# Kernel tuning notes

Measured on AMD Instinct MI355X. Metric: run time of the kernel, lower is better.

## Reference

```python
import jax, jax.numpy as jnp
import numpy as np

N = 102400   # nodes (256 graphs x 400 nodes)
E = 819200   # edges (avg degree 8)
D = 120      # input_channels
H = 200      # hidden_channels
CC = D + H   # 320 concat dim
L = 400      # nodes per graph (hardcoded view in forward)
B = N // L   # 256 graphs
STEPS = 8
NETYPES = 2


def conv1d(x, w, b):
    # x: [B, C, L], w: [O, I, K] -> [B, O, L-K+1] (VALID, like torch Conv1d)
    y = jax.lax.conv_general_dilated(x, w, (1,), 'VALID',
                                     dimension_numbers=('NCH', 'OIH', 'NCH'))
    return y + b[None, :, None]


def maxpool1d(x, k, s):
    return jax.lax.reduce_window(x, -jnp.inf, jax.lax.max,
                                 (1, 1, k), (1, 1, s), 'VALID')


def setup_inputs():
    key = jax.random.key(0)
    ks = jax.random.split(key, 32)
    g = lambda i, shape, s=0.05: jax.random.normal(ks[i], shape, jnp.float32) * s
    return dict(
        x=g(0, (N, D), 1.0),
        edge_index=jax.random.randint(ks[1], (2, E), 0, N),
        edge_types=jax.random.randint(ks[2], (E,), 0, NETYPES),
        ggnn_W=g(3, (NETYPES, H, H)), ggnn_b=g(4, (NETYPES, H)),
        gru_Wih=g(5, (3 * H, H)), gru_Whh=g(6, (3 * H, H)),
        gru_bih=g(7, (3 * H,)), gru_bhh=g(8, (3 * H,)),
        conv1_w=g(9, (H, H, 3)), conv1_b=g(10, (H,)),
        conv2_w=g(11, (H, H, 1)), conv2_b=g(12, (H,)),
        cconv1_w=g(13, (CC, CC, 3)), cconv1_b=g(14, (CC,)),
        cconv2_w=g(15, (CC, CC, 1)), cconv2_b=g(16, (CC,)),
        mlp_y_w=g(17, (256, H)), mlp_y_b=g(18, (256,)),
        mlp_z_w=g(19, (256, CC)), mlp_z_b=g(20, (256,)),
        ml_l1_w=g(21, (128, 256)), ml_l1_b=g(22, (128,)),
        ml_f1_w=g(23, (64, 128)), ml_f1_b=g(24, (64,)),
        ml_f2_w=g(25, (128, 64)), ml_f2_b=g(26, (128,)),
        cls_w=g(27, (2, 128)), cls_b=g(28, (2,)),
    )


def reference(x, edge_index, edge_types, ggnn_W, ggnn_b, gru_Wih, gru_Whh,
              gru_bih, gru_bhh, conv1_w, conv1_b, conv2_w, conv2_b,
              cconv1_w, cconv1_b, cconv2_w, cconv2_b, mlp_y_w, mlp_y_b,
              mlp_z_w, mlp_z_b, ml_l1_w, ml_l1_b, ml_f1_w, ml_f1_b,
              ml_f2_w, ml_f2_b, cls_w, cls_b):
    src, dst = edge_index[0], edge_index[1]
    emask = [(edge_types == e).astype(x.dtype)[:, None] for e in range(NETYPES)]

    # --- GatedGraphConv: zero-pad feats to H, then 8 steps of
    #     per-etype linear -> gather(src) -> scatter-add(dst) -> GRUCell ---
    h = jnp.pad(x, ((0, 0), (0, H - D)))  # [N, H]
    for _ in range(STEPS):
        a = jnp.zeros((N, H), x.dtype)
        for e in range(NETYPES):
            Wh = h @ ggnn_W[e].T + ggnn_b[e]           # [N, H]
            msg = Wh[src] * emask[e]                    # [E, H]
            a = a + jax.ops.segment_sum(msg, dst, num_segments=N)
        gi = a @ gru_Wih.T + gru_bih                    # [N, 3H]
        gh = h @ gru_Whh.T + gru_bhh                    # [N, 3H]
        ir, iz, inn = jnp.split(gi, 3, axis=-1)
        hr, hz, hn = jnp.split(gh, 3, axis=-1)
        r = jax.nn.sigmoid(ir + hr)
        z = jax.nn.sigmoid(iz + hz)
        n = jnp.tanh(inn + r * hn)
        h = (1.0 - z) * n + z * h
    outputs = h                                         # [N, H]

    # --- conv/pool readout (dropout = identity at eval) ---
    c_i = jnp.concatenate([x, outputs], axis=1).reshape(B, L, CC)
    h_i = outputs.reshape(B, L, H)

    Y1 = maxpool1d(jax.nn.relu(conv1d(h_i.transpose(0, 2, 1), conv1_w, conv1_b)), 3, 2)
    Y2 = maxpool1d(jax.nn.relu(conv1d(Y1, conv2_w, conv2_b)), 2, 2).transpose(0, 2, 1)  # [B,99,H]
    Z1 = maxpool1d(jax.nn.relu(conv1d(c_i.transpose(0, 2, 1), cconv1_w, cconv1_b)), 3, 2)
    Z2 = maxpool1d(jax.nn.relu(conv1d(Z1, cconv2_w, cconv2_b)), 2, 2).transpose(0, 2, 1)  # [B,99,CC]

    before_avg = (Y2 @ mlp_y_w.T + mlp_y_b) * (Z2 @ mlp_z_w.T + mlp_z_b)  # [B,99,256]
    avg = before_avg.mean(axis=1)                                          # [B,256]

    # --- MetricLearningModel head ---
    h1 = jax.nn.relu(avg @ ml_l1_w.T + ml_l1_b)                 # [B,128]
    hf = jax.nn.relu(h1 @ ml_f1_w.T + ml_f1_b)                  # [B,64]
    hf = jax.nn.relu(hf @ ml_f2_w.T + ml_f2_b)                  # [B,128] embedding
    logits = hf @ cls_w.T + cls_b                               # [B,2]
    return logits, hf
```

## Files before the change

kernel.cpp:

```cpp
#include <hip/hip_runtime.h>
#include <hip/hip_bf16.h>
#include <cstdint>
#include <cstddef>

static constexpr int NN = 102400;
static constexpr int EE = 819200;
static constexpr int DD = 120;
static constexpr int HH = 200;
static constexpr int LL = 400;
static constexpr int BB = 256;
static constexpr int NSTEPS = 8;

typedef __attribute__((ext_vector_type(8))) short short8;
typedef __attribute__((ext_vector_type(4))) float f32x4;

__device__ __forceinline__ unsigned short f2bf(float f) {
  union { float f; unsigned u; } v; v.f = f;
  return (unsigned short)((v.u + 0x7fffu + ((v.u >> 16) & 1u)) >> 16);
}
__device__ __forceinline__ float bf2f(unsigned short s) {
  union { unsigned u; float f; } v; v.u = ((unsigned)s) << 16; return v.f;
}

template<int AMODE, int ASRC, int OBF, int RELU>
__global__ __launch_bounds__(256) void gemm_mfma(
    const void* __restrict__ Asrc, const float* __restrict__ X2,
    const short* __restrict__ WP, const float* __restrict__ bias,
    void* __restrict__ Cdst, int M, int Nout, int K, int KT)
{
  __shared__ short Asm[4096];
  __shared__ short Bsm[4096];
  const int tid = threadIdx.x;
  const int row0 = blockIdx.y * 128;
  const int col0 = blockIdx.x * 128;

  f32x4 acc[4][4];
#pragma unroll
  for (int mi = 0; mi < 4; mi++)
#pragma unroll
    for (int ni = 0; ni < 4; ni++) acc[mi][ni] = (f32x4){0.f, 0.f, 0.f, 0.f};

  const int r = tid & 15;
  const int kgl = (tid >> 4) & 3;
  const int ghalf = tid >> 6;
  const int w = tid >> 6, l = tid & 63;
  const int wr = w >> 1, wc = w & 1;

  for (int t = 0; t < KT; t++) {
#pragma unroll
    for (int half = 0; half < 2; half++) {
      const int g = ghalf + half * 4;
      int row = row0 + g * 16 + r;
      if (row >= M) row = M - 1;
      const int k0 = t * 32 + kgl * 8;
      short8 sv;
      if (AMODE == 0 && ASRC == 1) {
        if (k0 < K) {
          sv = *reinterpret_cast<const short8*>(
              (const unsigned short*)Asrc + (size_t)row * K + k0);
        } else {
#pragma unroll
          for (int j = 0; j < 8; j++) sv[j] = 0;
        }
      } else {
        const float* p = nullptr;
        bool ok = true;
        if (AMODE == 0) {
          if (k0 < K) p = (const float*)Asrc + (size_t)row * K + k0;
          else ok = false;
        } else if (AMODE == 1) {
          if (k0 < K) {
            const int b = row / 398, tt = row - b * 398;
            const int tap = k0 / 200, i0 = k0 - tap * 200;
            p = (const float*)Asrc + ((size_t)(b * 400 + tt + tap)) * 200 + i0;
          } else ok = false;
        } else {
          const int b = row / 398, tt = row - b * 398;
          const int tap = k0 / 320, c0 = k0 - tap * 320;
          const int node = b * 400 + tt + tap;
          if (c0 < 120) p = X2 + (size_t)node * 120 + c0;
          else p = (const float*)Asrc + (size_t)node * 200 + (c0 - 120);
        }
        float v[8];
        if (ok) {
          const float4 x0 = *reinterpret_cast<const float4*>(p);
          const float4 x1 = *reinterpret_cast<const float4*>(p + 4);
          v[0] = x0.x; v[1] = x0.y; v[2] = x0.z; v[3] = x0.w;
          v[4] = x1.x; v[5] = x1.y; v[6] = x1.z; v[7] = x1.w;
        } else {
#pragma unroll
          for (int j = 0; j < 8; j++) v[j] = 0.f;
        }
#pragma unroll
        for (int j = 0; j < 8; j++) sv[j] = (short)f2bf(v[j]);
      }
      *reinterpret_cast<short8*>(&Asm[(g * 64 + (tid & 63)) * 8]) = sv;
    }
    {
      const size_t wbase = ((size_t)blockIdx.x * KT + t) * 4096;
#pragma unroll
      for (int it = 0; it < 2; it++) {
        const int idx = it * 256 + tid;
        *reinterpret_cast<short8*>(&Bsm[idx * 8]) =
            *reinterpret_cast<const short8*>(WP + wbase + (size_t)idx * 8);
      }
    }
    __syncthreads();
    short8 af[4], bfr[4];
#pragma unroll
    for (int mi = 0; mi < 4; mi++)
      af[mi] = *reinterpret_cast<const short8*>(&Asm[((wr * 4 + mi) * 64 + l) * 8]);
#pragma unroll
    for (int ni = 0; ni < 4; ni++)
      bfr[ni] = *reinterpret_cast<const short8*>(&Bsm[((wc * 4 + ni) * 64 + l) * 8]);
#pragma unroll
    for (int mi = 0; mi < 4; mi++)
#pragma unroll
      for (int ni = 0; ni < 4; ni++)
        acc[mi][ni] = __builtin_amdgcn_mfma_f32_16x16x32_bf16(
            af[mi], bfr[ni], acc[mi][ni], 0, 0, 0);
    __syncthreads();
  }

#pragma unroll
  for (int mi = 0; mi < 4; mi++)
#pragma unroll
    for (int ni = 0; ni < 4; ni++) {
      const int col = col0 + wc * 64 + ni * 16 + (l & 15);
      if (col < Nout) {
        const float bb = bias ? bias[col] : 0.f;
        const int rbase = row0 + wr * 64 + mi * 16 + ((l >> 4) << 2);
#pragma unroll
        for (int q = 0; q < 4; q++) {
          const int row = rbase + q;
          if (row < M) {
            float val = acc[mi][ni][q] + bb;
            if (RELU) val = fmaxf(val, 0.f);
            if (OBF)
              ((unsigned short*)Cdst)[(size_t)row * Nout + col] = f2bf(val);
            else
              ((float*)Cdst)[(size_t)row * Nout + col] = val;
          }
        }
      }
    }
}

__global__ void pack_w(const float* __restrict__ W, short* __restrict__ WP,
                       int Nout, int K, int Ntp, int Kp, int CIN) {
  const int KT = Kp >> 5;
  const int total = (Ntp >> 7) * KT * 512;
  const int u = blockIdx.x * 256 + threadIdx.x;
  if (u >= total) return;
  const int l = u & 63;
  const int g = (u >> 6) & 7;
  const int T = (u >> 9) % KT;
  const int ct = (u >> 9) / KT;
  const int n = ct * 128 + g * 16 + (l & 15);
  const int kb = T * 32 + ((l >> 4) << 3);
  short8 sv;
#pragma unroll
  for (int j = 0; j < 8; j++) {
    const int k = kb + j;
    float v = 0.f;
    if (n < Nout && k < K) {
      if (CIN > 0) {
        const int kw = k / CIN, i = k - kw * CIN;
        v = W[((size_t)n * CIN + i) * 3 + kw];
      } else {
        v = W[(size_t)n * K + k];
      }
    }
    sv[j] = (short)f2bf(v);
  }
  *reinterpret_cast<short8*>(&WP[(size_t)u * 8]) = sv;
}

__global__ void fill_kernel(float* __restrict__ p, int n, float v) {
  const int t = blockIdx.x * 256 + threadIdx.x;
  if (t < n) p[t] = v;
}

__global__ void pad_h_kernel(const float* __restrict__ x, float* __restrict__ h) {
  const int t = blockIdx.x * 256 + threadIdx.x;
  if (t >= NN * HH) return;
  const int n = t / HH, j = t - n * HH;
  h[t] = (j < DD) ? x[(size_t)n * DD + j] : 0.0f;
}

__global__ void hist_kernel(const int* __restrict__ ei, int* __restrict__ cnt) {
  const int e = blockIdx.x * 256 + threadIdx.x;
  if (e < EE) atomicAdd(&cnt[ei[EE + e]], 1);
}
__global__ void scan1_kernel(const int* __restrict__ cnt, int* __restrict__ ex,
                             int* __restrict__ bsum) {
  __shared__ int sm[256];
  const int tid = threadIdx.x;
  const int i = blockIdx.x * 256 + tid;
  const int v = cnt[i];
  sm[tid] = v; __syncthreads();
  for (int off = 1; off < 256; off <<= 1) {
    int t = (tid >= off) ? sm[tid - off] : 0;
    __syncthreads();
    sm[tid] += t;
    __syncthreads();
  }
  ex[i] = sm[tid] - v;
  if (tid == 255) bsum[blockIdx.x] = sm[255];
}
__global__ void scan2_kernel(int* __restrict__ bsum, int nb) {
  if (threadIdx.x == 0 && blockIdx.x == 0) {
    int run = 0;
    for (int b = 0; b < nb; b++) { int t = bsum[b]; bsum[b] = run; run += t; }
  }
}
__global__ void scan3_kernel(const int* __restrict__ ex, const int* __restrict__ bsum,
                             int* __restrict__ rowptr) {
  const int i = blockIdx.x * 256 + threadIdx.x;
  if (i < NN) rowptr[i] = ex[i] + bsum[i >> 8];
  if (i == 0) rowptr[NN] = EE;
}
__global__ void fillcsr_kernel(const int* __restrict__ ei, const int* __restrict__ et,
                               const int* __restrict__ rowptr, int* __restrict__ fcur,
                               int* __restrict__ eidx) {
  const int e = blockIdx.x * 256 + threadIdx.x;
  if (e >= EE) return;
  const int d = ei[EE + e];
  const int pos = atomicAdd(&fcur[d], 1);
  eidx[rowptr[d] + pos] = (ei[e] << 1) | (et[e] & 1);
}

__global__ void agg_kernel(const unsigned short* __restrict__ Whb,
                           const int* __restrict__ rowptr,
                           const int* __restrict__ eidx,
                           const float* __restrict__ gb,
                           unsigned short* __restrict__ abf) {
  const int nid = blockIdx.x * 4 + (threadIdx.x >> 6);
  const int lane = threadIdx.x & 63;
  if (nid >= NN) return;
  const int beg = rowptr[nid], end = rowptr[nid + 1];
  float a0 = 0.f, a1 = 0.f, a2 = 0.f, a3 = 0.f, c0 = 0.f, c1 = 0.f;
  const unsigned int* W32 = (const unsigned int*)Whb;
  for (int e = beg; e < end; e++) {
    const int pe = eidx[e];
    const int src = pe >> 1, ty = pe & 1;
    if (ty) c1 += 1.f; else c0 += 1.f;
    const unsigned int* wrow = W32 + (size_t)src * 200 + ty * 100;
    const unsigned int u0 = wrow[lane];
    a0 += bf2f((unsigned short)(u0 & 0xffffu));
    a1 += bf2f((unsigned short)(u0 >> 16));
    if (lane < 36) {
      const unsigned int u1 = wrow[64 + lane];
      a2 += bf2f((unsigned short)(u1 & 0xffffu));
      a3 += bf2f((unsigned short)(u1 >> 16));
    }
  }
  unsigned int* A32 = (unsigned int*)abf;
  const int cA = 2 * lane, cB = cA + 1;
  a0 += c0 * gb[cA] + c1 * gb[200 + cA];
  a1 += c0 * gb[cB] + c1 * gb[200 + cB];
  A32[(size_t)nid * 100 + lane] =
      (unsigned int)f2bf(a0) | ((unsigned int)f2bf(a1) << 16);
  if (lane < 36) {
    const int cC = 128 + 2 * lane, cD = cC + 1;
    a2 += c0 * gb[cC] + c1 * gb[200 + cC];
    a3 += c0 * gb[cD] + c1 * gb[200 + cD];
    A32[(size_t)nid * 100 + 64 + lane] =
        (unsigned int)f2bf(a2) | ((unsigned int)f2bf(a3) << 16);
  }
}

__global__ void gru_kernel(const unsigned short* __restrict__ gi,
                           const unsigned short* __restrict__ gh,
                           float* __restrict__ h, int n0, int NC) {
  const int t = blockIdx.x * 256 + threadIdx.x;
  if (t >= NC * HH) return;
  const int ln = t / HH, j = t - ln * HH;
  const unsigned short* gir = gi + (size_t)ln * 600;
  const unsigned short* ghr = gh + (size_t)ln * 600;
  const float ir = bf2f(gir[j]), iz = bf2f(gir[200 + j]), inn = bf2f(gir[400 + j]);
  const float hr = bf2f(ghr[j]), hz = bf2f(ghr[200 + j]), hn = bf2f(ghr[400 + j]);
  const float rr = 1.0f / (1.0f + expf(-(ir + hr)));
  const float zz = 1.0f / (1.0f + expf(-(iz + hz)));
  const float nn = tanhf(inn + rr * hn);
  const size_t hi = (size_t)(n0 + ln) * HH + j;
  h[hi] = (1.0f - zz) * nn + zz * h[hi];
}

__global__ void pool_kernel(const float* __restrict__ src, float* __restrict__ dst,
                            int nb, int Lin, int Lout, int C, int win) {
  const size_t t = (size_t)blockIdx.x * 256 + threadIdx.x;
  const size_t tot = (size_t)nb * Lout * C;
  if (t >= tot) return;
  const int c = (int)(t % C);
  const size_t bp = t / C;
  const int p = (int)(bp % Lout);
  const int b = (int)(bp / Lout);
  const float* s0 = src + ((size_t)b * Lin + 2 * p) * C + c;
  float v = s0[0];
  for (int q = 1; q < win; q++) v = fmaxf(v, s0[(size_t)q * C]);
  dst[t] = v;
}

__global__ void prodmean_kernel(const float* __restrict__ y, const float* __restrict__ z,
                                float* __restrict__ avg, int g0, int nb) {
  const int t = blockIdx.x * 256 + threadIdx.x;
  if (t >= nb * 256) return;
  const int b = t >> 8, j = t & 255;
  const float* yr = y + (size_t)b * 99 * 256 + j;
  const float* zr = z + (size_t)b * 99 * 256 + j;
  float sum = 0.0f;
  for (int p = 0; p < 99; p++) sum += yr[(size_t)p * 256] * zr[(size_t)p * 256];
  avg[(size_t)(g0 + b) * 256 + j] = sum * (1.0f / 99.0f);
}

extern "C" void kernel_launch(void* const* d_in, const int* in_sizes, int n_in,
                              void* d_out, int out_size, void* d_ws, size_t ws_size,
                              hipStream_t stream) {
  const float* x       = (const float*)d_in[0];
  const int*   ei      = (const int*)d_in[1];
  const int*   et      = (const int*)d_in[2];
  const float* ggnn_W  = (const float*)d_in[3];
  const float* ggnn_b  = (const float*)d_in[4];
  const float* gru_Wih = (const float*)d_in[5];
  const float* gru_Whh = (const float*)d_in[6];
  const float* gru_bih = (const float*)d_in[7];
  const float* gru_bhh = (const float*)d_in[8];
  const float* conv1_w = (const float*)d_in[9];
  const float* conv1_b = (const float*)d_in[10];
  const float* conv2_w = (const float*)d_in[11];
  const float* conv2_b = (const float*)d_in[12];
  const float* cconv1_w = (const float*)d_in[13];
  const float* cconv1_b = (const float*)d_in[14];
  const float* cconv2_w = (const float*)d_in[15];
  const float* cconv2_b = (const float*)d_in[16];
  const float* mlp_y_w = (const float*)d_in[17];
  const float* mlp_y_b = (const float*)d_in[18];
  const float* mlp_z_w = (const float*)d_in[19];
  const float* mlp_z_b = (const float*)d_in[20];
  const float* ml_l1_w = (const float*)d_in[21];
  const float* ml_l1_b = (const float*)d_in[22];
  const float* ml_f1_w = (const float*)d_in[23];
  const float* ml_f1_b = (const float*)d_in[24];
  const float* ml_f2_w = (const float*)d_in[25];
  const float* ml_f2_b = (const float*)d_in[26];
  const float* cls_w   = (const float*)d_in[27];
  const float* cls_b   = (const float*)d_in[28];
  float* out = (float*)d_out;

  char* base = (char*)d_ws;
  size_t off = 0;
  auto alloc = [&](size_t bytes) { char* p = base + off; off += (bytes + 15) & ~(size_t)15; return p; };
  float* h            = (float*)alloc(81920000);
  unsigned short* abf = (unsigned short*)alloc(40960000);
  int* cnt    = (int*)alloc(409600);
  int* ex     = (int*)alloc(409600);
  int* bsum   = (int*)alloc(1600);
  int* rowptr = (int*)alloc(409604);
  int* fcur   = (int*)alloc(409600);
  int* eidx   = (int*)alloc(3276800);
  short* WPg   = (short*)alloc(229376);
  short* WPwih = (short*)alloc(286720);
  short* WPwhh = (short*)alloc(286720);
  short* WPc1  = (short*)alloc(311296);
  short* WPcc1 = (short*)alloc(737280);
  short* WPc2  = (short*)alloc(114688);
  short* WPcc2 = (short*)alloc(245760);
  short* WPmy  = (short*)alloc(114688);
  short* WPmz  = (short*)alloc(163840);
  short* WPl1  = (short*)alloc(65536);
  short* WPf1  = (short*)alloc(32768);
  short* WPf2  = (short*)alloc(16384);
  short* WPcls = (short*)alloc(32768);
  float* avg = (float*)alloc(262144);
  float* h1b = (float*)alloc(131072);
  float* hf1 = (float*)alloc(65536);
  char* dynb = base + off;
  const size_t dyn_bytes = (ws_size > off) ? (ws_size - off) : 0;

  const size_t WHB_BYTES = 81920000;
  int CH2 = (int)((dyn_bytes / 2400) & ~(size_t)127);
  if (CH2 > NN) CH2 = NN;
  int G = 0;
  { const int cand[4] = {256, 128, 64, 32};
    for (int i = 0; i < 4; i++)
      if ((size_t)cand[i] * 1222240 <= dyn_bytes) { G = cand[i]; break; } }

  const int fill_blocks = (out_size + 255) / 256;
  if (dyn_bytes < WHB_BYTES || CH2 < 128 || G == 0) {
    fill_kernel<<<fill_blocks, 256, 0, stream>>>(out, out_size,
                                                 -(float)(ws_size >> 20));
    return;
  }
  fill_kernel<<<fill_blocks, 256, 0, stream>>>(out, out_size, 1.0e4f);

  pad_h_kernel<<<80000, 256, 0, stream>>>(x, h);
  hipMemsetAsync(cnt, 0, 409600, stream);
  hipMemsetAsync(fcur, 0, 409600, stream);
  hist_kernel<<<3200, 256, 0, stream>>>(ei, cnt);
  scan1_kernel<<<400, 256, 0, stream>>>(cnt, ex, bsum);
  scan2_kernel<<<1, 64, 0, stream>>>(bsum, 400);
  scan3_kernel<<<400, 256, 0, stream>>>(ex, bsum, rowptr);
  fillcsr_kernel<<<3200, 256, 0, stream>>>(ei, et, rowptr, fcur, eidx);

  auto packs = [&](const float* W, short* WP, int Nout, int K, int Ntp, int Kp, int CIN) {
    const int total = (Ntp >> 7) * (Kp >> 5) * 512;
    pack_w<<<(total + 255) / 256, 256, 0, stream>>>(W, WP, Nout, K, Ntp, Kp, CIN);
  };
  packs(ggnn_W,  WPg,   400, 200, 512, 224, 0);
  packs(gru_Wih, WPwih, 600, 200, 640, 224, 0);
  packs(gru_Whh, WPwhh, 600, 200, 640, 224, 0);
  packs(conv1_w, WPc1,  200, 600, 256, 608, 200);
  packs(cconv1_w,WPcc1, 320, 960, 384, 960, 320);
  packs(conv2_w, WPc2,  200, 200, 256, 224, 0);
  packs(cconv2_w,WPcc2, 320, 320, 384, 320, 0);
  packs(mlp_y_w, WPmy,  256, 200, 256, 224, 0);
  packs(mlp_z_w, WPmz,  256, 320, 256, 320, 0);
  packs(ml_l1_w, WPl1,  128, 256, 128, 256, 0);
  packs(ml_f1_w, WPf1,   64, 128, 128, 128, 0);
  packs(ml_f2_w, WPf2,  128,  64, 128,  64, 0);
  packs(cls_w,   WPcls,   2, 128, 128, 128, 0);

  unsigned short* Whb = (unsigned short*)dynb;
  unsigned short* gi  = (unsigned short*)dynb;
  unsigned short* gh  = gi + (size_t)CH2 * 600;
  for (int step = 0; step < NSTEPS; step++) {
    gemm_mfma<0, 0, 1, 0><<<dim3(4, 800), 256, 0, stream>>>(
        h, nullptr, WPg, nullptr, Whb, NN, 400, 200, 7);
    agg_kernel<<<25600, 256, 0, stream>>>(Whb, rowptr, eidx, ggnn_b, abf);
    for (int n0 = 0; n0 < NN; n0 += CH2) {
      const int NC = (NN - n0 < CH2) ? (NN - n0) : CH2;
      const int gy = (NC + 127) / 128;
      gemm_mfma<0, 1, 1, 0><<<dim3(5, gy), 256, 0, stream>>>(
          abf + (size_t)n0 * HH, nullptr, WPwih, gru_bih, gi, NC, 600, 200, 7);
      gemm_mfma<0, 0, 1, 0><<<dim3(5, gy), 256, 0, stream>>>(
          h + (size_t)n0 * HH, nullptr, WPwhh, gru_bhh, gh, NC, 600, 200, 7);
      gru_kernel<<<(NC * HH + 255) / 256, 256, 0, stream>>>(gi, gh, h, n0, NC);
    }
  }

  float* b0  = (float*)dynb;
  float* b1  = b0 + (size_t)G * 127360;
  float* b2  = b1 + (size_t)G * 63360;
  float* y2c = b2 + (size_t)G * 63360;
  float* z2c = y2c + (size_t)G * 19800;

  for (int g0 = 0; g0 < BB; g0 += G) {
    const float* hc = h + (size_t)g0 * LL * HH;
    const float* xc = x + (size_t)g0 * LL * DD;
    const int M1 = G * 398, M2 = G * 198, M3 = G * 99;
    const int gy1 = (M1 + 127) / 128, gy2 = (M2 + 127) / 128, gy3 = (M3 + 127) / 128;
    gemm_mfma<1, 0, 0, 1><<<dim3(2, gy1), 256, 0, stream>>>(
        hc, nullptr, WPc1, conv1_b, b0, M1, 200, 600, 19);
    pool_kernel<<<(int)(((size_t)G * 198 * 200 + 255) / 256), 256, 0, stream>>>(
        b0, b1, G, 398, 198, 200, 3);
    gemm_mfma<0, 0, 0, 1><<<dim3(2, gy2), 256, 0, stream>>>(
        b1, nullptr, WPc2, conv2_b, b2, M2, 200, 200, 7);
    pool_kernel<<<(int)(((size_t)G * 99 * 200 + 255) / 256), 256, 0, stream>>>(
        b2, y2c, G, 198, 99, 200, 2);
    gemm_mfma<2, 0, 0, 1><<<dim3(3, gy1), 256, 0, stream>>>(
        hc, xc, WPcc1, cconv1_b, b0, M1, 320, 960, 30);
    pool_kernel<<<(int)(((size_t)G * 198 * 320 + 255) / 256), 256, 0, stream>>>(
        b0, b1, G, 398, 198, 320, 3);
    gemm_mfma<0, 0, 0, 1><<<dim3(3, gy2), 256, 0, stream>>>(
        b1, nullptr, WPcc2, cconv2_b, b2, M2, 320, 320, 10);
    pool_kernel<<<(int)(((size_t)G * 99 * 320 + 255) / 256), 256, 0, stream>>>(
        b2, z2c, G, 198, 99, 320, 2);
    gemm_mfma<0, 0, 0, 0><<<dim3(2, gy3), 256, 0, stream>>>(
        y2c, nullptr, WPmy, mlp_y_b, b0, M3, 256, 200, 7);
    gemm_mfma<0, 0, 0, 0><<<dim3(2, gy3), 256, 0, stream>>>(
        z2c, nullptr, WPmz, mlp_z_b, b1, M3, 256, 320, 10);
    prodmean_kernel<<<(G * 256 + 255) / 256, 256, 0, stream>>>(b0, b1, avg, g0, G);
  }

  gemm_mfma<0, 0, 0, 1><<<dim3(1, 2), 256, 0, stream>>>(
      avg, nullptr, WPl1, ml_l1_b, h1b, 256, 128, 256, 8);
  gemm_mfma<0, 0, 0, 1><<<dim3(1, 2), 256, 0, stream>>>(
      h1b, nullptr, WPf1, ml_f1_b, hf1, 256, 64, 128, 4);
  gemm_mfma<0, 0, 0, 1><<<dim3(1, 2), 256, 0, stream>>>(
      hf1, nullptr, WPf2, ml_f2_b, out + 512, 256, 128, 64, 2);
  gemm_mfma<0, 0, 0, 0><<<dim3(1, 2), 256, 0, stream>>>(
      out + 512, nullptr, WPcls, cls_b, out, 256, 2, 128, 4);
}
```

Before: 5.773 ms.

## Aggregate before transform and fuse GGNN+GRU into one GEMM with gated epilogue

```diff
diff --git a/kernel.cpp b/kernel.cpp
--- a/kernel.cpp
+++ b/kernel.cpp
@@ -22,11 +22,14 @@
   union { unsigned u; float f; } v; v.u = ((unsigned)s) << 16; return v.f;
 }
 
-template<int AMODE, int ASRC, int OBF, int RELU>
+template<int AMODE, int ASRC, int OBF, int RELU, int EPI>
 __global__ __launch_bounds__(256) void gemm_mfma(
-    const void* __restrict__ Asrc, const float* __restrict__ X2,
+    const void* __restrict__ Asrc, const void* __restrict__ A2,
     const short* __restrict__ WP, const float* __restrict__ bias,
-    void* __restrict__ Cdst, int M, int Nout, int K, int KT)
+    void* __restrict__ Cdst, int M, int Nout, int K, int KT,
+    const float* __restrict__ tt0, const float* __restrict__ tt1,
+    const float* __restrict__ cnt2, float* __restrict__ hout,
+    unsigned short* __restrict__ hbout)
 {
   __shared__ short Asm[4096];
   __shared__ short Bsm[4096];
@@ -54,45 +57,66 @@
       if (row >= M) row = M - 1;
       const int k0 = t * 32 + kgl * 8;
       short8 sv;
+      bool direct = false;
       if (AMODE == 0 && ASRC == 1) {
         if (k0 < K) {
           sv = *reinterpret_cast<const short8*>(
               (const unsigned short*)Asrc + (size_t)row * K + k0);
-        } else {
-#pragma unroll
-          for (int j = 0; j < 8; j++) sv[j] = 0;
-        }
-      } else {
-        const float* p = nullptr;
-        bool ok = true;
-        if (AMODE == 0) {
-          if (k0 < K) p = (const float*)Asrc + (size_t)row * K + k0;
-          else ok = false;
-        } else if (AMODE == 1) {
-          if (k0 < K) {
-            const int b = row / 398, tt = row - b * 398;
-            const int tap = k0 / 200, i0 = k0 - tap * 200;
-            p = (const float*)Asrc + ((size_t)(b * 400 + tt + tap)) * 200 + i0;
-          } else ok = false;
-        } else {
+          direct = true;
+        }
+      } else if (AMODE == 1) {
+        if (k0 < K) {
+          const int b = row / 398, tt = row - b * 398;
+          const int tap = k0 / 200, i0 = k0 - tap * 200;
+          sv = *reinterpret_cast<const short8*>(
+              (const unsigned short*)Asrc + ((size_t)(b * 400 + tt + tap)) * 200 + i0);
+          direct = true;
+        }
+      } else if (AMODE == 3) {
+        if (k0 < 400) {
+          sv = *reinterpret_cast<const short8*>(
+              (const unsigned short*)Asrc + (size_t)row * 400 + k0);
+          direct = true;
+        } else if (k0 < 600) {
+          sv = *reinterpret_cast<const short8*>(
+              (const unsigned short*)A2 + (size_t)row * 200 + (k0 - 400));
+          direct = true;
+        }
+      } else if (AMODE == 2) {
+        if (k0 < K) {
           const int b = row / 398, tt = row - b * 398;
           const int tap = k0 / 320, c0 = k0 - tap * 320;
           const int node = b * 400 + tt + tap;
-          if (c0 < 120) p = X2 + (size_t)node * 120 + c0;
-          else p = (const float*)Asrc + (size_t)node * 200 + (c0 - 120);
-        }
-        float v[8];
-        if (ok) {
+          if (c0 < 120) {
+            const float* p = (const float*)A2 + (size_t)node * 120 + c0;
+            const float4 x0 = *reinterpret_cast<const float4*>(p);
+            const float4 x1 = *reinterpret_cast<const float4*>(p + 4);
+            sv[0] = (short)f2bf(x0.x); sv[1] = (short)f2bf(x0.y);
+            sv[2] = (short)f2bf(x0.z); sv[3] = (short)f2bf(x0.w);
+            sv[4] = (short)f2bf(x1.x); sv[5] = (short)f2bf(x1.y);
+            sv[6] = (short)f2bf(x1.z); sv[7] = (short)f2bf(x1.w);
+            direct = true;
+          } else {
+            sv = *reinterpret_cast<const short8*>(
+                (const unsigned short*)Asrc + (size_t)node * 200 + (c0 - 120));
+            direct = true;
+          }
+        }
+      } else {
+        if (k0 < K) {
+          const float* p = (const float*)Asrc + (size_t)row * K + k0;
           const float4 x0 = *reinterpret_cast<const float4*>(p);
           const float4 x1 = *reinterpret_cast<const float4*>(p + 4);
-          v[0] = x0.x; v[1] = x0.y; v[2] = x0.z; v[3] = x0.w;
-          v[4] = x1.x; v[5] = x1.y; v[6] = x1.z; v[7] = x1.w;
-        } else {
-#pragma unroll
-          for (int j = 0; j < 8; j++) v[j] = 0.f;
-        }
-#pragma unroll
-        for (int j = 0; j < 8; j++) sv[j] = (short)f2bf(v[j]);
+          sv[0] = (short)f2bf(x0.x); sv[1] = (short)f2bf(x0.y);
+          sv[2] = (short)f2bf(x0.z); sv[3] = (short)f2bf(x0.w);
+          sv[4] = (short)f2bf(x1.x); sv[5] = (short)f2bf(x1.y);
+          sv[6] = (short)f2bf(x1.z); sv[7] = (short)f2bf(x1.w);
+          direct = true;
+        }
+      }
+      if (!direct) {
+#pragma unroll
+        for (int j = 0; j < 8; j++) sv[j] = 0;
       }
       *reinterpret_cast<short8*>(&Asm[(g * 64 + (tid & 63)) * 8]) = sv;
     }
@@ -122,28 +146,61 @@
     __syncthreads();
   }
 
-#pragma unroll
-  for (int mi = 0; mi < 4; mi++)
-#pragma unroll
-    for (int ni = 0; ni < 4; ni++) {
-      const int col = col0 + wc * 64 + ni * 16 + (l & 15);
-      if (col < Nout) {
-        const float bb = bias ? bias[col] : 0.f;
-        const int rbase = row0 + wr * 64 + mi * 16 + ((l >> 4) << 2);
-#pragma unroll
-        for (int q = 0; q < 4; q++) {
-          const int row = rbase + q;
-          if (row < M) {
-            float val = acc[mi][ni][q] + bb;
-            if (RELU) val = fmaxf(val, 0.f);
-            if (OBF)
-              ((unsigned short*)Cdst)[(size_t)row * Nout + col] = f2bf(val);
-            else
-              ((float*)Cdst)[(size_t)row * Nout + col] = val;
+  if (EPI == 0) {
+#pragma unroll
+    for (int mi = 0; mi < 4; mi++)
+#pragma unroll
+      for (int ni = 0; ni < 4; ni++) {
+        const int col = col0 + wc * 64 + ni * 16 + (l & 15);
+        if (col < Nout) {
+          const float bbv = bias ? bias[col] : 0.f;
+          const int rbase = row0 + wr * 64 + mi * 16 + ((l >> 4) << 2);
+#pragma unroll
+          for (int q = 0; q < 4; q++) {
+            const int row = rbase + q;
+            if (row < M) {
+              float val = acc[mi][ni][q] + bbv;
+              if (RELU) val = fmaxf(val, 0.f);
+              if (OBF)
+                ((unsigned short*)Cdst)[(size_t)row * Nout + col] = f2bf(val);
+              else
+                ((float*)Cdst)[(size_t)row * Nout + col] = val;
+            }
+          }
+        }
+      }
+  } else {
+    const int g = l & 3;
+#pragma unroll
+    for (int mi = 0; mi < 4; mi++) {
+#pragma unroll
+      for (int q = 0; q < 4; q++) {
+        const int row = row0 + wr * 64 + mi * 16 + ((l >> 4) << 2) + q;
+        const float2 cc = *reinterpret_cast<const float2*>(cnt2 + (size_t)row * 2);
+#pragma unroll
+        for (int ni = 0; ni < 4; ni++) {
+          const int col = col0 + wc * 64 + ni * 16 + (l & 15);
+          float val = acc[mi][ni][q] + bias[col] + cc.x * tt0[col] + cc.y * tt1[col];
+          float av;
+          if (g == 0 || g == 1) av = 1.f / (1.f + expf(-val));
+          else av = val;
+          const float x1 = __shfl_xor(av, 1);
+          const float x2 = __shfl_xor(av, 2);
+          const float x3 = __shfl_xor(av, 3);
+          if (g == 2 && col < 800) {
+            const int ch = col >> 2;
+            const float nv = tanhf(av + x2 * x1);
+            float hold;
+            if (hout) hold = hout[(size_t)row * 200 + ch];
+            else hold = bf2f(((const unsigned short*)A2)[(size_t)row * 200 + ch]);
+            const float hnew = (1.f - x3) * nv + x3 * hold;
+            if (hout) hout[(size_t)row * 200 + ch] = hnew;
+            hbout[(size_t)row * 200 + ch] = f2bf(hnew);
           }
         }
       }
     }
+  }
 }
 
 __global__ void pack_w(const float* __restrict__ W, short* __restrict__ WP,
@@ -181,11 +238,14 @@
   if (t < n) p[t] = v;
 }
 
-__global__ void pad_h_kernel(const float* __restrict__ x, float* __restrict__ h) {
+__global__ void pad_h_kernel(const float* __restrict__ x, float* __restrict__ h,
+                             unsigned short* __restrict__ hb) {
   const int t = blockIdx.x * 256 + threadIdx.x;
   if (t >= NN * HH) return;
   const int n = t / HH, j = t - n * HH;
-  h[t] = (j < DD) ? x[(size_t)n * DD + j] : 0.0f;
+  const float v = (j < DD) ? x[(size_t)n * DD + j] : 0.0f;
+  if (h) h[t] = v;
+  hb[t] = f2bf(v);
 }
 
 __global__ void hist_kernel(const int* __restrict__ ei, int* __restrict__ cnt) {
@@ -229,62 +289,94 @@
   const int pos = atomicAdd(&fcur[d], 1);
   eidx[rowptr[d] + pos] = (ei[e] << 1) | (et[e] & 1);
 }
-
-__global__ void agg_kernel(const unsigned short* __restrict__ Whb,
-                           const int* __restrict__ rowptr,
-                           const int* __restrict__ eidx,
-                           const float* __restrict__ gb,
-                           unsigned short* __restrict__ abf) {
+__global__ void count_kernel(const int* __restrict__ ei, const int* __restrict__ et,
+                             float* __restrict__ cnt2) {
+  const int e = blockIdx.x * 256 + threadIdx.x;
+  if (e >= EE) return;
+  atomicAdd(&cnt2[(size_t)ei[EE + e] * 2 + (et[e] & 1)], 1.0f);
+}
+
+__global__ void wcat2_kernel(const float* __restrict__ gw, float* __restrict__ W2) {
+  const int t = blockIdx.x * 256 + threadIdx.x;
+  if (t >= 400 * 200) return;
+  const int m = t / 200, j = t - m * 200;
+  const int ty = (m < 200) ? 0 : 1;
+  const int kk = m - ty * 200;
+  W2[t] = gw[(size_t)ty * 40000 + j * 200 + kk];
+}
+__global__ void ta_kernel(const float* __restrict__ wih, const float* __restrict__ gb,
+                          float* __restrict__ ta) {
+  const int o = blockIdx.x * 256 + threadIdx.x;
+  if (o >= 1200) return;
+  const int which = o / 600, oo = o - which * 600;
+  float s = 0.f;
+  for (int j = 0; j < 200; j++) s += wih[(size_t)oo * 200 + j] * gb[which * 200 + j];
+  ta[o] = s;
+}
+__global__ void wfd_kernel(const float* __restrict__ M1, const float* __restrict__ whh,
+                           float* __restrict__ WFD) {
+  const int t = blockIdx.x * 256 + threadIdx.x;
+  if (t >= 800 * 600) return;
+  const int c = t / 600, k = t - c * 600;
+  const int ch = c >> 2, g = c & 3;
+  float v = 0.f;
+  if (g == 0) v = (k < 400) ? M1[(size_t)ch * 400 + k] : whh[(size_t)ch * 200 + (k - 400)];
+  else if (g == 1) v = (k < 400) ? M1[(size_t)(200 + ch) * 400 + k]
+                                 : whh[(size_t)(200 + ch) * 200 + (k - 400)];
+  else if (g == 2) v = (k < 400) ? M1[(size_t)(400 + ch) * 400 + k] : 0.f;
+  else v = (k < 400) ? 0.f : whh[(size_t)(400 + ch) * 200 + (k - 400)];
+  WFD[t] = v;
+}
+__global__ void bbtt_kernel(const float* __restrict__ bih, const float* __restrict__ bhh,
+                            const float* __restrict__ ta, float* __restrict__ bb,
+                            float* __restrict__ tt0, float* __restrict__ tt1) {
+  const int c = blockIdx.x * 256 + threadIdx.x;
+  if (c >= 896) return;
+  const int ch = c >> 2, g = c & 3;
+  float b = 0.f, t0 = 0.f, t1 = 0.f;
+  if (ch < 200) {
+    if (g == 0) b = bih[ch] + bhh[ch];
+    else if (g == 1) b = bih[200 + ch] + bhh[200 + ch];
+    else if (g == 2) b = bih[400 + ch];
+    else b = bhh[400 + ch];
+    if (g < 3) { t0 = ta[g * 200 + ch]; t1 = ta[600 + g * 200 + ch]; }
+  }
+  bb[c] = b; tt0[c] = t0; tt1[c] = t1;
+}
+
+__global__ void gather_kernel(const unsigned short* __restrict__ hb,
+                              const int* __restrict__ rowptr,
+                              const int* __restrict__ eidx,
+                              unsigned short* __restrict__ s) {
   const int nid = blockIdx.x * 4 + (threadIdx.x >> 6);
-  const int lane = threadIdx.x & 63;
+  const int l = threadIdx.x & 63;
   if (nid >= NN) return;
   const int beg = rowptr[nid], end = rowptr[nid + 1];
-  float a0 = 0.f, a1 = 0.f, a2 = 0.f, a3 = 0.f, c0 = 0.f, c1 = 0.f;
-  const unsigned int* W32 = (const unsigned int*)Whb;
+  float a00 = 0, a01 = 0, a10 = 0, a11 = 0;
+  float b00 = 0, b01 = 0, b10 = 0, b11 = 0;
+  const unsigned int* H32 = (const unsigned int*)hb;
   for (int e = beg; e < end; e++) {
     const int pe = eidx[e];
     const int src = pe >> 1, ty = pe & 1;
-    if (ty) c1 += 1.f; else c0 += 1.f;
-    const unsigned int* wrow = W32 + (size_t)src * 200 + ty * 100;
-    const unsigned int u0 = wrow[lane];
-    a0 += bf2f((unsigned short)(u0 & 0xffffu));
-    a1 += bf2f((unsigned short)(u0 >> 16));
-    if (lane < 36) {
-      const unsigned int u1 = wrow[64 + lane];
-      a2 += bf2f((unsigned short)(u1 & 0xffffu));
-      a3 += bf2f((unsigned short)(u1 >> 16));
-    }
-  }
-  unsigned int* A32 = (unsigned int*)abf;
-  const int cA = 2 * lane, cB = cA + 1;
-  a0 += c0 * gb[cA] + c1 * gb[200 + cA];
-  a1 += c0 * gb[cB] + c1 * gb[200 + cB];
-  A32[(size_t)nid * 100 + lane] =
-      (unsigned int)f2bf(a0) | ((unsigned int)f2bf(a1) << 16);
-  if (lane < 36) {
-    const int cC = 128 + 2 * lane, cD = cC + 1;
-    a2 += c0 * gb[cC] + c1 * gb[200 + cC];
-    a3 += c0 * gb[cD] + c1 * gb[200 + cD];
-    A32[(size_t)nid * 100 + 64 + lane] =
-        (unsigned int)f2bf(a2) | ((unsigned int)f2bf(a3) << 16);
-  }
-}
-
-__global__ void gru_kernel(const unsigned short* __restrict__ gi,
-                           const unsigned short* __restrict__ gh,
-                           float* __restrict__ h, int n0, int NC) {
-  const int t = blockIdx.x * 256 + threadIdx.x;
-  if (t >= NC * HH) return;
-  const int ln = t / HH, j = t - ln * HH;
-  const unsigned short* gir = gi + (size_t)ln * 600;
-  const unsigned short* ghr = gh + (size_t)ln * 600;
-  const float ir = bf2f(gir[j]), iz = bf2f(gir[200 + j]), inn = bf2f(gir[400 + j]);
-  const float hr = bf2f(ghr[j]), hz = bf2f(ghr[200 + j]), hn = bf2f(ghr[400 + j]);
-  const float rr = 1.0f / (1.0f + expf(-(ir + hr)));
-  const float zz = 1.0f / (1.0f + expf(-(iz + hz)));
-  const float nn = tanhf(inn + rr * hn);
-  const size_t hi = (size_t)(n0 + ln) * HH + j;
-  h[hi] = (1.0f - zz) * nn + zz * h[hi];
+    const unsigned int* hr = H32 + (size_t)src * 100;
+    const unsigned int u0 = hr[l];
+    unsigned int u1 = 0;
+    if (l < 36) u1 = hr[64 + l];
+    const float f0 = bf2f((unsigned short)(u0 & 0xffffu));
+    const float f1 = bf2f((unsigned short)(u0 >> 16));
+    const float f2 = bf2f((unsigned short)(u1 & 0xffffu));
+    const float f3 = bf2f((unsigned short)(u1 >> 16));
+    if (ty == 0) { a00 += f0; a01 += f1; a10 += f2; a11 += f3; }
+    else         { b00 += f0; b01 += f1; b10 += f2; b11 += f3; }
+  }
+  unsigned int* S32 = (unsigned int*)s;
+  const size_t rb = (size_t)nid * 200;
+  S32[rb + l] = (unsigned int)f2bf(a00) | ((unsigned int)f2bf(a01) << 16);
+  S32[rb + 100 + l] = (unsigned int)f2bf(b00) | ((unsigned int)f2bf(b01) << 16);
+  if (l < 36) {
+    S32[rb + 64 + l] = (unsigned int)f2bf(a10) | ((unsigned int)f2bf(a11) << 16);
+    S32[rb + 164 + l] = (unsigned int)f2bf(b10) | ((unsigned int)f2bf(b11) << 16);
+  }
 }
 
 __global__ void pool_kernel(const float* __restrict__ src, float* __restrict__ dst,
@@ -351,17 +443,14 @@
   char* base = (char*)d_ws;
   size_t off = 0;
   auto alloc = [&](size_t bytes) { char* p = base + off; off += (bytes + 15) & ~(size_t)15; return p; };
-  float* h            = (float*)alloc(81920000);
-  unsigned short* abf = (unsigned short*)alloc(40960000);
-  int* cnt    = (int*)alloc(409600);
-  int* ex     = (int*)alloc(409600);
-  int* bsum   = (int*)alloc(1600);
-  int* rowptr = (int*)alloc(409604);
-  int* fcur   = (int*)alloc(409600);
-  int* eidx   = (int*)alloc(3276800);
-  short* WPg   = (short*)alloc(229376);
-  short* WPwih = (short*)alloc(286720);
-  short* WPwhh = (short*)alloc(286720);
+  unsigned short* s   = (unsigned short*)alloc(81920000);
+  unsigned short* hb1 = (unsigned short*)alloc(40960000);
+  unsigned short* hb0 = (unsigned short*)alloc(40960000);
+  int* eidx    = (int*)alloc(3276800);
+  int* rowptr  = (int*)alloc(409604);
+  float* cnt2  = (float*)alloc(819200);
+  short* WPF   = (short*)alloc(1089536);
+  short* WPwc  = (short*)alloc(229376);
   short* WPc1  = (short*)alloc(311296);
   short* WPcc1 = (short*)alloc(737280);
   short* WPc2  = (short*)alloc(114688);
@@ -372,44 +461,60 @@
   short* WPf1  = (short*)alloc(32768);
   short* WPf2  = (short*)alloc(16384);
   short* WPcls = (short*)alloc(32768);
+  float* bb  = (float*)alloc(3584);
+  float* tt0 = (float*)alloc(3584);
+  float* tt1 = (float*)alloc(3584);
   float* avg = (float*)alloc(262144);
   float* h1b = (float*)alloc(131072);
   float* hf1 = (float*)alloc(65536);
-  char* dynb = base + off;
-  const size_t dyn_bytes = (ws_size > off) ? (ws_size - off) : 0;
-
-  const size_t WHB_BYTES = 81920000;
-  int CH2 = (int)((dyn_bytes / 2400) & ~(size_t)127);
-  if (CH2 > NN) CH2 = NN;
-  int G = 0;
-  { const int cand[4] = {256, 128, 64, 32};
-    for (int i = 0; i < 4; i++)
-      if ((size_t)cand[i] * 1222240 <= dyn_bytes) { G = cand[i]; break; } }
+  const size_t persist = off;
+  float* h = (float*)alloc(81920000);
+  const bool has_h = (ws_size >= off);
 
   const int fill_blocks = (out_size + 255) / 256;
-  if (dyn_bytes < WHB_BYTES || CH2 < 128 || G == 0) {
+  if (ws_size < persist) {
     fill_kernel<<<fill_blocks, 256, 0, stream>>>(out, out_size,
                                                  -(float)(ws_size >> 20));
     return;
   }
+  float* hptr = has_h ? h : nullptr;
+
+  char* ali = (char*)s;
+  float* Wcat2 = (float*)(ali);
+  float* M1f   = (float*)(ali + 320000);
+  float* WFD   = (float*)(ali + 1280000);
+  float* ta    = (float*)(ali + 3200000);
+  int* cnt     = (int*)(ali + 3204800);
+  int* ex      = (int*)(ali + 3614400);
+  int* bsum    = (int*)(ali + 4024000);
+  int* fcur    = (int*)(ali + 4025600);
+
   fill_kernel<<<fill_blocks, 256, 0, stream>>>(out, out_size, 1.0e4f);
 
-  pad_h_kernel<<<80000, 256, 0, stream>>>(x, h);
+  pad_h_kernel<<<80000, 256, 0, stream>>>(x, hptr, hb0);
   hipMemsetAsync(cnt, 0, 409600, stream);
   hipMemsetAsync(fcur, 0, 409600, stream);
+  hipMemsetAsync(cnt2, 0, 819200, stream);
   hist_kernel<<<3200, 256, 0, stream>>>(ei, cnt);
   scan1_kernel<<<400, 256, 0, stream>>>(cnt, ex, bsum);
   scan2_kernel<<<1, 64, 0, stream>>>(bsum, 400);
   scan3_kernel<<<400, 256, 0, stream>>>(ex, bsum, rowptr);
   fillcsr_kernel<<<3200, 256, 0, stream>>>(ei, et, rowptr, fcur, eidx);
+  count_kernel<<<3200, 256, 0, stream>>>(ei, et, cnt2);
 
   auto packs = [&](const float* W, short* WP, int Nout, int K, int Ntp, int Kp, int CIN) {
     const int total = (Ntp >> 7) * (Kp >> 5) * 512;
     pack_w<<<(total + 255) / 256, 256, 0, stream>>>(W, WP, Nout, K, Ntp, Kp, CIN);
   };
-  packs(ggnn_W,  WPg,   400, 200, 512, 224, 0);
-  packs(gru_Wih, WPwih, 600, 200, 640, 224, 0);
-  packs(gru_Whh, WPwhh, 600, 200, 640, 224, 0);
+  wcat2_kernel<<<313, 256, 0, stream>>>(ggnn_W, Wcat2);
+  packs(Wcat2, WPwc, 400, 200, 512, 224, 0);
+  gemm_mfma<0, 0, 0, 0, 0><<<dim3(4, 5), 256, 0, stream>>>(
+      gru_Wih, nullptr, WPwc, nullptr, M1f, 600, 400, 200, 7,
+      nullptr, nullptr, nullptr, nullptr, nullptr);
+  ta_kernel<<<5, 256, 0, stream>>>(gru_Wih, ggnn_b, ta);
+  wfd_kernel<<<1875, 256, 0, stream>>>(M1f, gru_Whh, WFD);
+  packs(WFD, WPF, 800, 600, 896, 608, 0);
+  bbtt_kernel<<<4, 256, 0, stream>>>(gru_bih, gru_bhh, ta, bb, tt0, tt1);
   packs(conv1_w, WPc1,  200, 600, 256, 608, 200);
   packs(cconv1_w,WPcc1, 320, 960, 384, 960, 320);
   packs(conv2_w, WPc2,  200, 200, 256, 224, 0);
@@ -421,64 +526,67 @@
   packs(ml_f2_w, WPf2,  128,  64, 128,  64, 0);
   packs(cls_w,   WPcls,   2, 128, 128, 128, 0);
 
-  unsigned short* Whb = (unsigned short*)dynb;
-  unsigned short* gi  = (unsigned short*)dynb;
-  unsigned short* gh  = gi + (size_t)CH2 * 600;
+  unsigned short* hbb[2] = {hb0, hb1};
   for (int step = 0; step < NSTEPS; step++) {
-    gemm_mfma<0, 0, 1, 0><<<dim3(4, 800), 256, 0, stream>>>(
-        h, nullptr, WPg, nullptr, Whb, NN, 400, 200, 7);
-    agg_kernel<<<25600, 256, 0, stream>>>(Whb, rowptr, eidx, ggnn_b, abf);
-    for (int n0 = 0; n0 < NN; n0 += CH2) {
-      const int NC = (NN - n0 < CH2) ? (NN - n0) : CH2;
-      const int gy = (NC + 127) / 128;
-      gemm_mfma<0, 1, 1, 0><<<dim3(5, gy), 256, 0, stream>>>(
-          abf + (size_t)n0 * HH, nullptr, WPwih, gru_bih, gi, NC, 600, 200, 7);
-      gemm_mfma<0, 0, 1, 0><<<dim3(5, gy), 256, 0, stream>>>(
-          h + (size_t)n0 * HH, nullptr, WPwhh, gru_bhh, gh, NC, 600, 200, 7);
-      gru_kernel<<<(NC * HH + 255) / 256, 256, 0, stream>>>(gi, gh, h, n0, NC);
-    }
-  }
-
-  float* b0  = (float*)dynb;
+    unsigned short* hcur = hbb[step & 1];
+    unsigned short* hnxt = hbb[(step & 1) ^ 1];
+    gather_kernel<<<25600, 256, 0, stream>>>(hcur, rowptr, eidx, s);
+    gemm_mfma<3, 1, 0, 0, 2><<<dim3(7, 800), 256, 0, stream>>>(
+        s, hcur, WPF, bb, nullptr, NN, 896, 600, 19,
+        tt0, tt1, cnt2, hptr, hnxt);
+  }
+
+  const int G = 64;
+  float* b0  = (float*)s;
   float* b1  = b0 + (size_t)G * 127360;
   float* b2  = b1 + (size_t)G * 63360;
   float* y2c = b2 + (size_t)G * 63360;
   float* z2c = y2c + (size_t)G * 19800;
 
   for (int g0 = 0; g0 < BB; g0 += G) {
-    const float* hc = h + (size_t)g0 * LL * HH;
+    const unsigned short* hc = hb0 + (size_t)g0 * LL * HH;
     const float* xc = x + (size_t)g0 * LL * DD;
     const int M1 = G * 398, M2 = G * 198, M3 = G * 99;
     const int gy1 = (M1 + 127) / 128, gy2 = (M2 + 127) / 128, gy3 = (M3 + 127) / 128;
-    gemm_mfma<1, 0, 0, 1><<<dim3(2, gy1), 256, 0, stream>>>(
-        hc, nullptr, WPc1, conv1_b, b0, M1, 200, 600, 19);
+    gemm_mfma<1, 1, 0, 1, 0><<<dim3(2, gy1), 256, 0, stream>>>(
+        hc, nullptr, WPc1, conv1_b, b0, M1, 200, 600, 19,
+        nullptr, nullptr, nullptr, nullptr, nullptr);
     pool_kernel<<<(int)(((size_t)G * 198 * 200 + 255) / 256), 256, 0, stream>>>(
         b0, b1, G, 398, 198, 200, 3);
-    gemm_mfma<0, 0, 0, 1><<<dim3(2, gy2), 256, 0, stream>>>(
-        b1, nullptr, WPc2, conv2_b, b2, M2, 200, 200, 7);
+    gemm_mfma<0, 0, 0, 1, 0><<<dim3(2, gy2), 256, 0, stream>>>(
+        b1, nullptr, WPc2, conv2_b, b2, M2, 200, 200, 7,
+        nullptr, nullptr, nullptr, nullptr, nullptr);
     pool_kernel<<<(int)(((size_t)G * 99 * 200 + 255) / 256), 256, 0, stream>>>(
         b2, y2c, G, 198, 99, 200, 2);
-    gemm_mfma<2, 0, 0, 1><<<dim3(3, gy1), 256, 0, stream>>>(
-        hc, xc, WPcc1, cconv1_b, b0, M1, 320, 960, 30);
+    gemm_mfma<2, 1, 0, 1, 0><<<dim3(3, gy1), 256, 0, stream>>>(
+        hc, xc, WPcc1, cconv1_b, b0, M1, 320, 960, 30,
+        nullptr, nullptr, nullptr, nullptr, nullptr);
     pool_kernel<<<(int)(((size_t)G * 198 * 320 + 255) / 256), 256, 0, stream>>>(
         b0, b1, G, 398, 198, 320, 3);
-    gemm_mfma<0, 0, 0, 1><<<dim3(3, gy2), 256, 0, stream>>>(
-        b1, nullptr, WPcc2, cconv2_b, b2, M2, 320, 320, 10);
+    gemm_mfma<0, 0, 0, 1, 0><<<dim3(3, gy2), 256, 0, stream>>>(
+        b1, nullptr, WPcc2, cconv2_b, b2, M2, 320, 320, 10,
+        nullptr, nullptr, nullptr, nullptr, nullptr);
     pool_kernel<<<(int)(((size_t)G * 99 * 320 + 255) / 256), 256, 0, stream>>>(
         b2, z2c, G, 198, 99, 320, 2);
-    gemm_mfma<0, 0, 0, 0><<<dim3(2, gy3), 256, 0, stream>>>(
-        y2c, nullptr, WPmy, mlp_y_b, b0, M3, 256, 200, 7);
-    gemm_mfma<0, 0, 0, 0><<<dim3(2, gy3), 256, 0, stream>>>(
-        z2c, nullptr, WPmz, mlp_z_b, b1, M3, 256, 320, 10);
+    gemm_mfma<0, 0, 0, 0, 0><<<dim3(2, gy3), 256, 0, stream>>>(
+        y2c, nullptr, WPmy, mlp_y_b, b0, M3, 256, 200, 7,
+        nullptr, nullptr, nullptr, nullptr, nullptr);
+    gemm_mfma<0, 0, 0, 0, 0><<<dim3(2, gy3), 256, 0, stream>>>(
+        z2c, nullptr, WPmz, mlp_z_b, b1, M3, 256, 320, 10,
+        nullptr, nullptr, nullptr, nullptr, nullptr);
     prodmean_kernel<<<(G * 256 + 255) / 256, 256, 0, stream>>>(b0, b1, avg, g0, G);
   }
 
-  gemm_mfma<0, 0, 0, 1><<<dim3(1, 2), 256, 0, stream>>>(
-      avg, nullptr, WPl1, ml_l1_b, h1b, 256, 128, 256, 8);
-  gemm_mfma<0, 0, 0, 1><<<dim3(1, 2), 256, 0, stream>>>(
-      h1b, nullptr, WPf1, ml_f1_b, hf1, 256, 64, 128, 4);
-  gemm_mfma<0, 0, 0, 1><<<dim3(1, 2), 256, 0, stream>>>(
-      hf1, nullptr, WPf2, ml_f2_b, out + 512, 256, 128, 64, 2);
-  gemm_mfma<0, 0, 0, 0><<<dim3(1, 2), 256, 0, stream>>>(
-      out + 512, nullptr, WPcls, cls_b, out, 256, 2, 128, 4);
-}
+  gemm_mfma<0, 0, 0, 1, 0><<<dim3(1, 2), 256, 0, stream>>>(
+      avg, nullptr, WPl1, ml_l1_b, h1b, 256, 128, 256, 8,
+      nullptr, nullptr, nullptr, nullptr, nullptr);
+  gemm_mfma<0, 0, 0, 1, 0><<<dim3(1, 2), 256, 0, stream>>>(
+      h1b, nullptr, WPf1, ml_f1_b, hf1, 256, 64, 128, 4,
+      nullptr, nullptr, nullptr, nullptr, nullptr);
+  gemm_mfma<0, 0, 0, 1, 0><<<dim3(1, 2), 256, 0, stream>>>(
+      hf1, nullptr, WPf2, ml_f2_b, out + 512, 256, 128, 64, 2,
+      nullptr, nullptr, nullptr, nullptr, nullptr);
+  gemm_mfma<0, 0, 0, 0, 0><<<dim3(1, 2), 256, 0, stream>>>(
+      out + 512, nullptr, WPcls, cls_b, out, 256, 2, 128, 4,
+      nullptr, nullptr, nullptr, nullptr, nullptr);
+}
```

Measured after the change: 5.957 ms. +3.2%, slower.
